# Optimization experiments

Hardware: AMD Instinct MI355X
Metric: run time of the kernel (lower is better)

## Reference

```python
import jax, jax.numpy as jnp
import numpy as np

DIM = 192
HRES, WRES = 64, 64
NUM_HEADS = 6
WS = 8  # window_size
MLP_HIDDEN = int(DIM * 4.0)
EPS = 1e-5


def layer_norm(x, gamma, beta):
    mu = jnp.mean(x, axis=-1, keepdims=True)
    var = jnp.var(x, axis=-1, keepdims=True)
    return (x - mu) * jax.lax.rsqrt(var + EPS) * gamma + beta


def window_partition(x, ws):
    B, H, W, C = x.shape
    x = x.reshape(B, H // ws, ws, W // ws, ws, C)
    x = jnp.transpose(x, (0, 1, 3, 2, 4, 5))
    return x.reshape(-1, ws * ws, C)


def window_reverse(windows, ws, H, W, C):
    B = windows.shape[0] // ((H // ws) * (W // ws))
    x = windows.reshape(B, H // ws, W // ws, ws, ws, C)
    x = jnp.transpose(x, (0, 1, 3, 2, 4, 5))
    return x.reshape(B, H, W, C)


def setup_inputs() -> dict:
    key = jax.random.key(0)
    ks = jax.random.split(key, 12)
    s = 0.02
    return {
        "x": jax.random.normal(ks[0], (32, HRES * WRES, DIM), dtype=jnp.float32),
        "norm1_g": jnp.ones((DIM,), jnp.float32),
        "norm1_b": jnp.zeros((DIM,), jnp.float32),
        "qkv_w": jax.random.normal(ks[1], (DIM, 3 * DIM), jnp.float32) * s,
        "qkv_b": jnp.zeros((3 * DIM,), jnp.float32),
        "proj_w": jax.random.normal(ks[2], (DIM, DIM), jnp.float32) * s,
        "proj_b": jnp.zeros((DIM,), jnp.float32),
        "norm2_g": jnp.ones((DIM,), jnp.float32),
        "norm2_b": jnp.zeros((DIM,), jnp.float32),
        "fc1_w": jax.random.normal(ks[3], (DIM, MLP_HIDDEN), jnp.float32) * s,
        "fc1_b": jnp.zeros((MLP_HIDDEN,), jnp.float32),
        "fc2_w": jax.random.normal(ks[4], (MLP_HIDDEN, DIM), jnp.float32) * s,
        "fc2_b": jnp.zeros((DIM,), jnp.float32),
    }


def reference(x, norm1_g, norm1_b, qkv_w, qkv_b, proj_w, proj_b,
              norm2_g, norm2_b, fc1_w, fc1_b, fc2_w, fc2_b):
    B, L, C = x.shape
    H, W = HRES, WRES
    hd = C // NUM_HEADS
    scale = hd ** -0.5

    shortcut = x
    h = layer_norm(x, norm1_g, norm1_b).reshape(B, H, W, C)
    win = window_partition(h, WS)  # [nW*B, WS*WS, C]
    Bw, N, _ = win.shape

    qkv = (win @ qkv_w + qkv_b).reshape(Bw, N, 3, NUM_HEADS, hd)
    q, k, v = jnp.transpose(qkv, (2, 0, 3, 1, 4))  # each [Bw, H, N, hd]
    attn = jnp.einsum('bhnd,bhmd->bhnm', q, k) * scale
    attn = jax.nn.softmax(attn, axis=-1)
    out = jnp.einsum('bhnm,bhmd->bhnd', attn, v)
    out = jnp.transpose(out, (0, 2, 1, 3)).reshape(Bw, N, C)
    out = out @ proj_w + proj_b

    h = window_reverse(out, WS, H, W, C).reshape(B, L, C)
    x = shortcut + h

    m = layer_norm(x, norm2_g, norm2_b)
    m = jax.nn.gelu(m @ fc1_w + fc1_b, approximate=False)
    m = m @ fc2_w + fc2_b
    return x + m
```

## Files before the change

### kernel.cpp

```cpp
#include <hip/hip_runtime.h>
#include <hip/hip_bf16.h>
#include <math.h>

#define DIM   192
#define NH    6
#define HD    32
#define WSZ   8
#define HRES_ 64
#define WRES_ 64
#define BATCH 32
#define LTOK  (HRES_*WRES_)
#define MTOK  (BATCH*LTOK)
#define QKVN  (3*DIM)
#define MLPH  (4*DIM)

using bf16 = __hip_bfloat16;
using bf16x8 = __attribute__((ext_vector_type(8))) short;
using f32x4  = __attribute__((ext_vector_type(4))) float;

__device__ __forceinline__ float bf2f(bf16 h) { return __bfloat162float(h); }
__device__ __forceinline__ float us2f(unsigned short u) {
    union { unsigned u32; float f; } c; c.u32 = ((unsigned)u) << 16; return c.f;
}

__global__ void detect_kernel(const unsigned short* __restrict__ g, int* __restrict__ flag)
{
    *flag = (g[0] == 0x3F80) ? 0 : 1;
}

__global__ __launch_bounds__(256) void cvt_kernel(
    const void* __restrict__ src, bf16* __restrict__ dst,
    long n, long elem_off, const int* __restrict__ flag)
{
    long i = ((long)blockIdx.x * 256 + threadIdx.x) * 8;
    if (i >= n) return;
    if (i + 8 <= n) {
        if (*flag) {
            const float* s = (const float*)src + elem_off + i;
            float4 a = *reinterpret_cast<const float4*>(s);
            float4 b = *reinterpret_cast<const float4*>(s + 4);
            bf16 o[8];
            o[0]=__float2bfloat16(a.x); o[1]=__float2bfloat16(a.y);
            o[2]=__float2bfloat16(a.z); o[3]=__float2bfloat16(a.w);
            o[4]=__float2bfloat16(b.x); o[5]=__float2bfloat16(b.y);
            o[6]=__float2bfloat16(b.z); o[7]=__float2bfloat16(b.w);
            *reinterpret_cast<bf16x8*>(dst + i) = *reinterpret_cast<const bf16x8*>(o);
        } else {
            *reinterpret_cast<bf16x8*>(dst + i) =
                *reinterpret_cast<const bf16x8*>((const bf16*)src + elem_off + i);
        }
    } else {
        for (long k2 = i; k2 < n; ++k2) {
            if (*flag) dst[k2] = __float2bfloat16(((const float*)src)[elem_off + k2]);
            else       dst[k2] = ((const bf16*)src)[elem_off + k2];
        }
    }
}

__global__ __launch_bounds__(256) void store_kernel(
    const bf16* __restrict__ src, void* __restrict__ dst,
    long n, long elem_off, const int* __restrict__ flag)
{
    long i = ((long)blockIdx.x * 256 + threadIdx.x) * 8;
    if (i >= n) return;
    if (i + 8 <= n) {
        bf16x8 v = *reinterpret_cast<const bf16x8*>(src + i);
        if (*flag) {
            float* d = (float*)dst + elem_off + i;
            float4 a, b;
            a.x = us2f((unsigned short)v[0]); a.y = us2f((unsigned short)v[1]);
            a.z = us2f((unsigned short)v[2]); a.w = us2f((unsigned short)v[3]);
            b.x = us2f((unsigned short)v[4]); b.y = us2f((unsigned short)v[5]);
            b.z = us2f((unsigned short)v[6]); b.w = us2f((unsigned short)v[7]);
            *reinterpret_cast<float4*>(d)     = a;
            *reinterpret_cast<float4*>(d + 4) = b;
        } else {
            *reinterpret_cast<bf16x8*>((bf16*)dst + elem_off + i) = v;
        }
    } else {
        for (long k2 = i; k2 < n; ++k2) {
            if (*flag) ((float*)dst)[elem_off + k2] = bf2f(src[k2]);
            else       ((bf16*)dst)[elem_off + k2] = src[k2];
        }
    }
}

__global__ __launch_bounds__(256) void ln_kernel(
    const bf16* __restrict__ x, const bf16* __restrict__ g,
    const bf16* __restrict__ b, bf16* __restrict__ y)
{
    int wave = threadIdx.x >> 6;
    int lane = threadIdx.x & 63;
    long token = (long)blockIdx.x * 4 + wave;
    const bf16* xp = x + token * DIM;
    float f0 = bf2f(xp[lane]);
    float f1 = bf2f(xp[lane + 64]);
    float f2 = bf2f(xp[lane + 128]);
    float s  = f0 + f1 + f2;
    float ss = f0*f0 + f1*f1 + f2*f2;
    #pragma unroll
    for (int m = 1; m < 64; m <<= 1) { s += __shfl_xor(s, m); ss += __shfl_xor(ss, m); }
    float mean = s * (1.0f/192.0f);
    float var  = ss * (1.0f/192.0f) - mean*mean;
    float rstd = rsqrtf(var + 1e-5f);
    bf16* yp = y + token * DIM;
    yp[lane]       = __float2bfloat16((f0-mean)*rstd*bf2f(g[lane])       + bf2f(b[lane]));
    yp[lane + 64]  = __float2bfloat16((f1-mean)*rstd*bf2f(g[lane + 64])  + bf2f(b[lane + 64]));
    yp[lane + 128] = __float2bfloat16((f2-mean)*rstd*bf2f(g[lane + 128]) + bf2f(b[lane + 128]));
}

__global__ void transpose_kernel(const bf16* __restrict__ in, bf16* __restrict__ out,
                                 int K, int N)
{
    int idx = blockIdx.x * 256 + threadIdx.x;
    if (idx < K * N) {
        int n = idx % N, k = idx / N;
        out[n * K + k] = in[idx];
    }
}

template<int EPI>
__global__ __launch_bounds__(256) void gemm_bt(
    const bf16* __restrict__ A, const bf16* __restrict__ Bt,
    const bf16* __restrict__ bias, const bf16* __restrict__ res,
    bf16* __restrict__ C, int M, int N, int K)
{
    constexpr int KC = 192;
    __shared__ __align__(16) bf16 bsh[(KC/32) * 4 * 64 * 8];
    int tid  = threadIdx.x;
    int wave = tid >> 6, lane = tid & 63;
    int t = lane & 15, q = lane >> 4;
    int  n0 = blockIdx.x * 64;
    long m0 = (long)blockIdx.y * 128;

    f32x4 acc[2][4] = {};

    for (int kc = 0; kc < K; kc += KC) {
        __syncthreads();
        for (int s = tid; s < (KC/32) * 256; s += 256) {
            int ks  = s >> 8;
            int rem = s & 255;
            int j   = rem >> 6;
            int ln  = rem & 63;
            int tt = ln & 15, qq = ln >> 4;
            int n = j * 16 + tt;
            int k = ks * 32 + qq * 8;
            const float4* src = reinterpret_cast<const float4*>(
                Bt + (long)(n0 + n) * K + kc + k);
            reinterpret_cast<float4*>(bsh)[s] = *src;
        }
        __syncthreads();

        const bf16* arow = A + (m0 + wave * 32 + t) * (long)K + kc + q * 8;
        #pragma unroll
        for (int ks = 0; ks < KC/32; ++ks) {
            bf16x8 a0 = *reinterpret_cast<const bf16x8*>(arow + ks * 32);
            bf16x8 a1 = *reinterpret_cast<const bf16x8*>(arow + 16 * (long)K + ks * 32);
            #pragma unroll
            for (int j = 0; j < 4; ++j) {
                bf16x8 b = reinterpret_cast<const bf16x8*>(bsh)[ks * 256 + j * 64 + lane];
                acc[0][j] = __builtin_amdgcn_mfma_f32_16x16x32_bf16(a0, b, acc[0][j], 0, 0, 0);
                acc[1][j] = __builtin_amdgcn_mfma_f32_16x16x32_bf16(a1, b, acc[1][j], 0, 0, 0);
            }
        }
    }

    #pragma unroll
    for (int j = 0; j < 4; ++j) {
        int col = n0 + j * 16 + t;
        float bv = bf2f(bias[col]);
        #pragma unroll
        for (int i = 0; i < 2; ++i) {
            #pragma unroll
            for (int r = 0; r < 4; ++r) {
                long row = m0 + wave * 32 + i * 16 + q * 4 + r;
                float v = acc[i][j][r] + bv;
                if (EPI == 1) v = v * 0.5f * (1.0f + erff(v * 0.70710678118f));
                if (EPI == 2) v += bf2f(res[row * N + col]);
                C[row * N + col] = __float2bfloat16(v);
            }
        }
    }
}

__global__ __launch_bounds__(256) void mlp_kernel(
    const bf16* __restrict__ A,   const bf16* __restrict__ W1t,
    const bf16* __restrict__ b1,  const bf16* __restrict__ W2t,
    const bf16* __restrict__ b2,  const bf16* __restrict__ res,
    bf16* __restrict__ out, int M)
{
    constexpr int HS = 88;
    __shared__ __align__(16) bf16 bsh[1536 * 8];
    __shared__ __align__(16) bf16 hsh[128 * HS];
    int tid  = threadIdx.x;
    int wave = tid >> 6, lane = tid & 63;
    int t = lane & 15, q = lane >> 4;
    long m0 = (long)blockIdx.x * 128;

    bf16x8 a_reg[2][6];
    #pragma unroll
    for (int i = 0; i < 2; ++i) {
        const bf16* ap = A + (m0 + wave * 32 + i * 16 + t) * (long)DIM + q * 8;
        #pragma unroll
        for (int ks = 0; ks < 6; ++ks)
            a_reg[i][ks] = *reinterpret_cast<const bf16x8*>(ap + ks * 32);
    }

    f32x4 oacc[2][12] = {};

    for (int nc = 0; nc < 12; ++nc) {
        __syncthreads();
        #pragma unroll
        for (int it = 0; it < 6; ++it) {
            int s   = it * 256 + tid;
            int ks  = s >> 8;
            int rem = s & 255;
            int j   = rem >> 6;
            int ln  = rem & 63;
            int n   = nc * 64 + j * 16 + (ln & 15);
            int k   = ks * 32 + (ln >> 4) * 8;
            reinterpret_cast<float4*>(bsh)[s] =
                *reinterpret_cast<const float4*>(W1t + (long)n * DIM + k);
        }
        __syncthreads();

        f32x4 hacc[2][4] = {};
        #pragma unroll
        for (int ks = 0; ks < 6; ++ks) {
            #pragma unroll
            for (int j = 0; j < 4; ++j) {
                bf16x8 b = reinterpret_cast<const bf16x8*>(bsh)[ks * 256 + j * 64 + lane];
                hacc[0][j] = __builtin_amdgcn_mfma_f32_16x16x32_bf16(a_reg[0][ks], b, hacc[0][j], 0, 0, 0);
                hacc[1][j] = __builtin_amdgcn_mfma_f32_16x16x32_bf16(a_reg[1][ks], b, hacc[1][j], 0, 0, 0);
            }
        }
        #pragma unroll
        for (int j = 0; j < 4; ++j) {
            float bv = bf2f(b1[nc * 64 + j * 16 + t]);
            #pragma unroll
            for (int i = 0; i < 2; ++i) {
                #pragma unroll
                for (int r = 0; r < 4; ++r) {
                    int row = wave * 32 + i * 16 + q * 4 + r;
                    float v = hacc[i][j][r] + bv;
                    v = v * 0.5f * (1.0f + erff(v * 0.70710678118f));
                    hsh[row * HS + j * 16 + t] = __float2bfloat16(v);
                }
            }
        }
        __syncthreads();

        #pragma unroll
        for (int it = 0; it < 6; ++it) {
            int s   = it * 256 + tid;
            int ks  = s / 768;
            int rem = s - ks * 768;
            int j   = rem >> 6;
            int ln  = rem & 63;
            int n   = j * 16 + (ln & 15);
            int k   = nc * 64 + ks * 32 + (ln >> 4) * 8;
            reinterpret_cast<float4*>(bsh)[s] =
                *reinterpret_cast<const float4*>(W2t + (long)n * MLPH + k);
        }
        __syncthreads();

        #pragma unroll
        for (int ks = 0; ks < 2; ++ks) {
            bf16x8 h0 = *reinterpret_cast<const bf16x8*>(hsh + (wave * 32 + t) * HS + ks * 32 + q * 8);
            bf16x8 h1 = *reinterpret_cast<const bf16x8*>(hsh + (wave * 32 + 16 + t) * HS + ks * 32 + q * 8);
            #pragma unroll
            for (int j = 0; j < 12; ++j) {
                bf16x8 b = reinterpret_cast<const bf16x8*>(bsh)[ks * 768 + j * 64 + lane];
                oacc[0][j] = __builtin_amdgcn_mfma_f32_16x16x32_bf16(h0, b, oacc[0][j], 0, 0, 0);
                oacc[1][j] = __builtin_amdgcn_mfma_f32_16x16x32_bf16(h1, b, oacc[1][j], 0, 0, 0);
            }
        }
    }

    #pragma unroll
    for (int j = 0; j < 12; ++j) {
        int col = j * 16 + t;
        float bv = bf2f(b2[col]);
        #pragma unroll
        for (int i = 0; i < 2; ++i) {
            #pragma unroll
            for (int r = 0; r < 4; ++r) {
                long row = m0 + wave * 32 + i * 16 + q * 4 + r;
                float v = oacc[i][j][r] + bv + bf2f(res[row * DIM + col]);
                out[row * DIM + col] = __float2bfloat16(v);
            }
        }
    }
}

__global__ __launch_bounds__(256) void attn_kernel(
    const bf16* __restrict__ qkv, bf16* __restrict__ out)
{
    int win  = blockIdx.x;
    int head = blockIdx.y;
    __shared__ __align__(16) bf16 qs[64 * 32];
    __shared__ __align__(16) bf16 ksm[64 * 32];
    __shared__ __align__(16) bf16 vt[32 * 64];
    __shared__ __align__(16) bf16 ps[64 * 64];
    __shared__ int nat[64];

    int tid  = threadIdx.x;
    int wave = tid >> 6, lane = tid & 63;
    int t = lane & 15, q = lane >> 4;

    if (tid < 64) {
        int b = win >> 6;
        int widx = win & 63;
        int wh = widx >> 3, ww = widx & 7;
        int r = wh * 8 + (tid >> 3);
        int c = ww * 8 + (tid & 7);
        nat[tid] = b * LTOK + r * WRES_ + c;
    }
    __syncthreads();

    {
        int token = tid >> 2, ch = tid & 3;
        long base = (long)nat[token] * QKVN + head * HD + ch * 8;
        float4 qv = *reinterpret_cast<const float4*>(qkv + base);
        float4 kv = *reinterpret_cast<const float4*>(qkv + base + DIM);
        float4 vv = *reinterpret_cast<const float4*>(qkv + base + 2 * DIM);
        *reinterpret_cast<float4*>(qs  + token * 32 + ch * 8) = qv;
        *reinterpret_cast<float4*>(ksm + token * 32 + ch * 8) = kv;
        const bf16* vp = reinterpret_cast<const bf16*>(&vv);
        #pragma unroll
        for (int e = 0; e < 8; ++e) vt[(ch * 8 + e) * 64 + token] = vp[e];
    }
    __syncthreads();

    f32x4 sacc[4] = {};
    {
        bf16x8 aq = *reinterpret_cast<const bf16x8*>(qs + (wave * 16 + t) * 32 + q * 8);
        #pragma unroll
        for (int j = 0; j < 4; ++j) {
            bf16x8 bk = *reinterpret_cast<const bf16x8*>(ksm + (j * 16 + t) * 32 + q * 8);
            sacc[j] = __builtin_amdgcn_mfma_f32_16x16x32_bf16(aq, bk, sacc[j], 0, 0, 0);
        }
    }

    const float scale = 0.17677669529663689f;
    #pragma unroll
    for (int r = 0; r < 4; ++r) {
        float m_ = fmaxf(fmaxf(sacc[0][r], sacc[1][r]), fmaxf(sacc[2][r], sacc[3][r]));
        #pragma unroll
        for (int msk = 1; msk < 16; msk <<= 1) m_ = fmaxf(m_, __shfl_xor(m_, msk));
        float p[4], sum = 0.f;
        #pragma unroll
        for (int j = 0; j < 4; ++j) { p[j] = expf((sacc[j][r] - m_) * scale); sum += p[j]; }
        #pragma unroll
        for (int msk = 1; msk < 16; msk <<= 1) sum += __shfl_xor(sum, msk);
        float inv = 1.0f / sum;
        int row = wave * 16 + q * 4 + r;
        #pragma unroll
        for (int j = 0; j < 4; ++j)
            ps[row * 64 + j * 16 + t] = __float2bfloat16(p[j] * inv);
    }
    __syncthreads();

    f32x4 oacc[2] = {};
    #pragma unroll
    for (int kk = 0; kk < 2; ++kk) {
        bf16x8 ap = *reinterpret_cast<const bf16x8*>(ps + (wave * 16 + t) * 64 + kk * 32 + q * 8);
        #pragma unroll
        for (int j = 0; j < 2; ++j) {
            bf16x8 bv = *reinterpret_cast<const bf16x8*>(vt + (j * 16 + t) * 64 + kk * 32 + q * 8);
            oacc[j] = __builtin_amdgcn_mfma_f32_16x16x32_bf16(ap, bv, oacc[j], 0, 0, 0);
        }
    }
    #pragma unroll
    for (int j = 0; j < 2; ++j) {
        #pragma unroll
        for (int r = 0; r < 4; ++r) {
            int row = wave * 16 + q * 4 + r;
            out[(long)nat[row] * DIM + head * HD + j * 16 + t] = __float2bfloat16(oacc[j][r]);
        }
    }
}

extern "C" void kernel_launch(void* const* d_in, const int* in_sizes, int n_in,
                              void* d_out, int out_size, void* d_ws, size_t ws_size,
                              hipStream_t stream)
{
    char* ws = (char*)d_ws;
    size_t off = 0;
    auto alloc = [&](size_t bytes) {
        char* p = ws + off;
        off += (bytes + 255) & ~(size_t)255;
        return p;
    };

    int* flag = (int*)alloc(sizeof(int));

    static const int psz[12] = { DIM, DIM, DIM*QKVN, QKVN, DIM*DIM, DIM,
                                 DIM, DIM, DIM*MLPH, MLPH, MLPH*DIM, DIM };
    bf16* par[12];
    for (int i = 0; i < 12; ++i) par[i] = (bf16*)alloc((size_t)psz[i] * 2);
    bf16 *n1g = par[0], *n1b = par[1], *qkvw = par[2], *qkvb = par[3],
         *projw = par[4], *projb = par[5], *n2g = par[6], *n2b = par[7],
         *fc1w = par[8], *fc1b = par[9], *fc2w = par[10], *fc2b = par[11];

    bf16* wqkv_t  = (bf16*)alloc((size_t)QKVN * DIM * 2);
    bf16* wproj_t = (bf16*)alloc((size_t)DIM * DIM * 2);
    bf16* wfc1_t  = (bf16*)alloc((size_t)MLPH * DIM * 2);
    bf16* wfc2_t  = (bf16*)alloc((size_t)DIM * MLPH * 2);
    size_t fixed_off = off;

    int C = 32;
    while (C > 1) {
        size_t Mc = (size_t)C * LTOK;
        if (fixed_off + Mc * 2304 + 4096 <= ws_size) break;
        C >>= 1;
    }
    size_t Mc = (size_t)C * LTOK;
    bf16* xb = (bf16*)alloc(Mc * 384);
    bf16* R  = (bf16*)alloc(Mc * 384);
    bf16* Y  = (bf16*)alloc(Mc * 384);
    bf16* S  = (bf16*)alloc(Mc * 1152);
    int nchunks = BATCH / C;

    detect_kernel<<<1, 1, 0, stream>>>((const unsigned short*)d_in[1], flag);

    for (int i = 0; i < 12; ++i) {
        unsigned blocks = (unsigned)(((long)psz[i] + 8*256 - 1) / (8*256));
        cvt_kernel<<<blocks, 256, 0, stream>>>(d_in[i + 1], par[i], psz[i], 0, flag);
    }

    transpose_kernel<<<(DIM*QKVN + 255)/256, 256, 0, stream>>>(qkvw, wqkv_t, DIM, QKVN);
    transpose_kernel<<<(DIM*DIM  + 255)/256, 256, 0, stream>>>(projw, wproj_t, DIM, DIM);
    transpose_kernel<<<(DIM*MLPH + 255)/256, 256, 0, stream>>>(fc1w, wfc1_t, DIM, MLPH);
    transpose_kernel<<<(MLPH*DIM + 255)/256, 256, 0, stream>>>(fc2w, wfc2_t, MLPH, DIM);

    for (int ci = 0; ci < nchunks; ++ci) {
        long eoff = (long)ci * Mc * DIM;
        long nelem = (long)Mc * DIM;
        unsigned vblocks = (unsigned)((nelem + 8*256 - 1) / (8*256));

        cvt_kernel<<<vblocks, 256, 0, stream>>>(d_in[0], xb, nelem, eoff, flag);
        ln_kernel<<<(unsigned)(Mc/4), 256, 0, stream>>>(xb, n1g, n1b, R);
        gemm_bt<0><<<dim3(QKVN/64, Mc/128), 256, 0, stream>>>(R, wqkv_t, qkvb, nullptr, S, (int)Mc, QKVN, DIM);
        attn_kernel<<<dim3(C*64, NH), 256, 0, stream>>>(S, R);
        gemm_bt<2><<<dim3(DIM/64, Mc/128), 256, 0, stream>>>(R, wproj_t, projb, xb, Y, (int)Mc, DIM, DIM);
        ln_kernel<<<(unsigned)(Mc/4), 256, 0, stream>>>(Y, n2g, n2b, R);
        mlp_kernel<<<(unsigned)(Mc/128), 256, 0, stream>>>(R, wfc1_t, fc1b, wfc2_t, fc2b, Y, Y, (int)Mc);
        store_kernel<<<vblocks, 256, 0, stream>>>(Y, d_out, nelem, eoff, flag);
    }
}
```

Measured before the change: 791.9 us.

## Halve MLP kernel row tile to 64 rows for higher occupancy

The fused MLP kernel now processes 64 rows per block instead of 128, each wave handling one 16-row MFMA tile instead of two. Accumulators, A registers and the hidden shared buffer shrink, and launch bounds request 3 blocks per CU, aiming to raise occupancy and latency hiding. In exchange, each block reloads the full fc1/fc2 weights for half as many rows, doubling weight traffic through shared memory and halving MFMA reuse per B-fragment load.

New measurement: 714.4 us. 1.11x faster.

```diff
diff --git a/kernel.cpp b/kernel.cpp
--- a/kernel.cpp
+++ b/kernel.cpp
@@ -183,7 +183,7 @@
     }
 }
 
-__global__ __launch_bounds__(256) void mlp_kernel(
+__global__ __launch_bounds__(256, 3) void mlp_kernel(
     const bf16* __restrict__ A,   const bf16* __restrict__ W1t,
     const bf16* __restrict__ b1,  const bf16* __restrict__ W2t,
     const bf16* __restrict__ b2,  const bf16* __restrict__ res,
@@ -191,22 +191,21 @@
 {
     constexpr int HS = 88;
     __shared__ __align__(16) bf16 bsh[1536 * 8];
-    __shared__ __align__(16) bf16 hsh[128 * HS];
+    __shared__ __align__(16) bf16 hsh[64 * HS];
     int tid  = threadIdx.x;
     int wave = tid >> 6, lane = tid & 63;
     int t = lane & 15, q = lane >> 4;
-    long m0 = (long)blockIdx.x * 128;
-
-    bf16x8 a_reg[2][6];
-    #pragma unroll
-    for (int i = 0; i < 2; ++i) {
-        const bf16* ap = A + (m0 + wave * 32 + i * 16 + t) * (long)DIM + q * 8;
+    long m0 = (long)blockIdx.x * 64;
+
+    bf16x8 a_reg[6];
+    {
+        const bf16* ap = A + (m0 + wave * 16 + t) * (long)DIM + q * 8;
         #pragma unroll
         for (int ks = 0; ks < 6; ++ks)
-            a_reg[i][ks] = *reinterpret_cast<const bf16x8*>(ap + ks * 32);
-    }
-
-    f32x4 oacc[2][12] = {};
+            a_reg[ks] = *reinterpret_cast<const bf16x8*>(ap + ks * 32);
+    }
+
+    f32x4 oacc[12] = {};
 
     for (int nc = 0; nc < 12; ++nc) {
         __syncthreads();
@@ -224,28 +223,24 @@
         }
         __syncthreads();
 
-        f32x4 hacc[2][4] = {};
+        f32x4 hacc[4] = {};
         #pragma unroll
         for (int ks = 0; ks < 6; ++ks) {
             #pragma unroll
             for (int j = 0; j < 4; ++j) {
                 bf16x8 b = reinterpret_cast<const bf16x8*>(bsh)[ks * 256 + j * 64 + lane];
-                hacc[0][j] = __builtin_amdgcn_mfma_f32_16x16x32_bf16(a_reg[0][ks], b, hacc[0][j], 0, 0, 0);
-                hacc[1][j] = __builtin_amdgcn_mfma_f32_16x16x32_bf16(a_reg[1][ks], b, hacc[1][j], 0, 0, 0);
+                hacc[j] = __builtin_amdgcn_mfma_f32_16x16x32_bf16(a_reg[ks], b, hacc[j], 0, 0, 0);
             }
         }
         #pragma unroll
         for (int j = 0; j < 4; ++j) {
             float bv = bf2f(b1[nc * 64 + j * 16 + t]);
             #pragma unroll
-            for (int i = 0; i < 2; ++i) {
-                #pragma unroll
-                for (int r = 0; r < 4; ++r) {
-                    int row = wave * 32 + i * 16 + q * 4 + r;
-                    float v = hacc[i][j][r] + bv;
-                    v = v * 0.5f * (1.0f + erff(v * 0.70710678118f));
-                    hsh[row * HS + j * 16 + t] = __float2bfloat16(v);
-                }
+            for (int r = 0; r < 4; ++r) {
+                int row = wave * 16 + q * 4 + r;
+                float v = hacc[j][r] + bv;
+                v = v * 0.5f * (1.0f + erff(v * 0.70710678118f));
+                hsh[row * HS + j * 16 + t] = __float2bfloat16(v);
             }
         }
         __syncthreads();
@@ -266,13 +261,11 @@
 
         #pragma unroll
         for (int ks = 0; ks < 2; ++ks) {
-            bf16x8 h0 = *reinterpret_cast<const bf16x8*>(hsh + (wave * 32 + t) * HS + ks * 32 + q * 8);
-            bf16x8 h1 = *reinterpret_cast<const bf16x8*>(hsh + (wave * 32 + 16 + t) * HS + ks * 32 + q * 8);
+            bf16x8 h = *reinterpret_cast<const bf16x8*>(hsh + (wave * 16 + t) * HS + ks * 32 + q * 8);
             #pragma unroll
             for (int j = 0; j < 12; ++j) {
                 bf16x8 b = reinterpret_cast<const bf16x8*>(bsh)[ks * 768 + j * 64 + lane];
-                oacc[0][j] = __builtin_amdgcn_mfma_f32_16x16x32_bf16(h0, b, oacc[0][j], 0, 0, 0);
-                oacc[1][j] = __builtin_amdgcn_mfma_f32_16x16x32_bf16(h1, b, oacc[1][j], 0, 0, 0);
+                oacc[j] = __builtin_amdgcn_mfma_f32_16x16x32_bf16(h, b, oacc[j], 0, 0, 0);
             }
         }
     }
@@ -282,13 +275,10 @@
         int col = j * 16 + t;
         float bv = bf2f(b2[col]);
         #pragma unroll
-        for (int i = 0; i < 2; ++i) {
-            #pragma unroll
-            for (int r = 0; r < 4; ++r) {
-                long row = m0 + wave * 32 + i * 16 + q * 4 + r;
-                float v = oacc[i][j][r] + bv + bf2f(res[row * DIM + col]);
-                out[row * DIM + col] = __float2bfloat16(v);
-            }
+        for (int r = 0; r < 4; ++r) {
+            long row = m0 + wave * 16 + q * 4 + r;
+            float v = oacc[j][r] + bv + bf2f(res[row * DIM + col]);
+            out[row * DIM + col] = __float2bfloat16(v);
         }
     }
 }
@@ -445,7 +435,7 @@
         attn_kernel<<<dim3(C*64, NH), 256, 0, stream>>>(S, R);
         gemm_bt<2><<<dim3(DIM/64, Mc/128), 256, 0, stream>>>(R, wproj_t, projb, xb, Y, (int)Mc, DIM, DIM);
         ln_kernel<<<(unsigned)(Mc/4), 256, 0, stream>>>(Y, n2g, n2b, R);
-        mlp_kernel<<<(unsigned)(Mc/128), 256, 0, stream>>>(R, wfc1_t, fc1b, wfc2_t, fc2b, Y, Y, (int)Mc);
+        mlp_kernel<<<(unsigned)(Mc/64), 256, 0, stream>>>(R, wfc1_t, fc1b, wfc2_t, fc2b, Y, Y, (int)Mc);
         store_kernel<<<vblocks, 256, 0, stream>>>(Y, d_out, nelem, eoff, flag);
     }
 }
```

## Split fused MLP block into 64-row tile with 2x2 wave grid

Applied to the files above, without the earlier changes.

Halves the fused MLP kernel's row tile from 128 to 64 and arranges the four waves as a 2x2 grid, so each wave computes half the hidden columns and half the output columns. This cuts the accumulator registers per wave (oacc drops from 24 to 12 vectors) and adds a launch bound asking for 3 blocks per SM, to raise occupancy and double the block count. In exchange, each fc1/fc2 weight tile staged in shared memory is reused across only 64 rows, which doubles total weight traffic from L2 into LDS.

Result: faster. 753.6 us (-4.8%).

```diff
diff --git a/kernel.cpp b/kernel.cpp
--- a/kernel.cpp
+++ b/kernel.cpp
@@ -22,6 +22,7 @@
 __device__ __forceinline__ float us2f(unsigned short u) {
     union { unsigned u32; float f; } c; c.u32 = ((unsigned)u) << 16; return c.f;
 }
+
 
 __global__ void detect_kernel(const unsigned short* __restrict__ g, int* __restrict__ flag)
 {
@@ -183,7 +184,7 @@
     }
 }
 
-__global__ __launch_bounds__(256) void mlp_kernel(
+__global__ __launch_bounds__(256, 3) void mlp_kernel(
     const bf16* __restrict__ A,   const bf16* __restrict__ W1t,
     const bf16* __restrict__ b1,  const bf16* __restrict__ W2t,
     const bf16* __restrict__ b2,  const bf16* __restrict__ res,
@@ -191,22 +192,23 @@
 {
     constexpr int HS = 88;
     __shared__ __align__(16) bf16 bsh[1536 * 8];
-    __shared__ __align__(16) bf16 hsh[128 * HS];
+    __shared__ __align__(16) bf16 hsh[64 * HS];
     int tid  = threadIdx.x;
     int wave = tid >> 6, lane = tid & 63;
     int t = lane & 15, q = lane >> 4;
-    long m0 = (long)blockIdx.x * 128;
+    int wr = wave >> 1, wc = wave & 1;
+    long m0 = (long)blockIdx.x * 64;
 
     bf16x8 a_reg[2][6];
     #pragma unroll
     for (int i = 0; i < 2; ++i) {
-        const bf16* ap = A + (m0 + wave * 32 + i * 16 + t) * (long)DIM + q * 8;
+        const bf16* ap = A + (m0 + wr * 32 + i * 16 + t) * (long)DIM + q * 8;
         #pragma unroll
         for (int ks = 0; ks < 6; ++ks)
             a_reg[i][ks] = *reinterpret_cast<const bf16x8*>(ap + ks * 32);
     }
 
-    f32x4 oacc[2][12] = {};
+    f32x4 oacc[2][6] = {};
 
     for (int nc = 0; nc < 12; ++nc) {
         __syncthreads();
@@ -224,27 +226,28 @@
         }
         __syncthreads();
 
-        f32x4 hacc[2][4] = {};
+        f32x4 hacc[2][2] = {};
         #pragma unroll
         for (int ks = 0; ks < 6; ++ks) {
-            #pragma unroll
-            for (int j = 0; j < 4; ++j) {
-                bf16x8 b = reinterpret_cast<const bf16x8*>(bsh)[ks * 256 + j * 64 + lane];
-                hacc[0][j] = __builtin_amdgcn_mfma_f32_16x16x32_bf16(a_reg[0][ks], b, hacc[0][j], 0, 0, 0);
-                hacc[1][j] = __builtin_amdgcn_mfma_f32_16x16x32_bf16(a_reg[1][ks], b, hacc[1][j], 0, 0, 0);
-            }
-        }
-        #pragma unroll
-        for (int j = 0; j < 4; ++j) {
-            float bv = bf2f(b1[nc * 64 + j * 16 + t]);
+            bf16x8 b0 = reinterpret_cast<const bf16x8*>(bsh)[ks * 256 + (wc * 2 + 0) * 64 + lane];
+            bf16x8 b1v = reinterpret_cast<const bf16x8*>(bsh)[ks * 256 + (wc * 2 + 1) * 64 + lane];
+            hacc[0][0] = __builtin_amdgcn_mfma_f32_16x16x32_bf16(a_reg[0][ks], b0,  hacc[0][0], 0, 0, 0);
+            hacc[0][1] = __builtin_amdgcn_mfma_f32_16x16x32_bf16(a_reg[0][ks], b1v, hacc[0][1], 0, 0, 0);
+            hacc[1][0] = __builtin_amdgcn_mfma_f32_16x16x32_bf16(a_reg[1][ks], b0,  hacc[1][0], 0, 0, 0);
+            hacc[1][1] = __builtin_amdgcn_mfma_f32_16x16x32_bf16(a_reg[1][ks], b1v, hacc[1][1], 0, 0, 0);
+        }
+        #pragma unroll
+        for (int j = 0; j < 2; ++j) {
+            int col = wc * 32 + j * 16 + t;
+            float bv = bf2f(b1[nc * 64 + col]);
             #pragma unroll
             for (int i = 0; i < 2; ++i) {
                 #pragma unroll
                 for (int r = 0; r < 4; ++r) {
-                    int row = wave * 32 + i * 16 + q * 4 + r;
+                    int row = wr * 32 + i * 16 + q * 4 + r;
                     float v = hacc[i][j][r] + bv;
                     v = v * 0.5f * (1.0f + erff(v * 0.70710678118f));
-                    hsh[row * HS + j * 16 + t] = __float2bfloat16(v);
+                    hsh[row * HS + col] = __float2bfloat16(v);
                 }
             }
         }
@@ -266,11 +269,11 @@
 
         #pragma unroll
         for (int ks = 0; ks < 2; ++ks) {
-            bf16x8 h0 = *reinterpret_cast<const bf16x8*>(hsh + (wave * 32 + t) * HS + ks * 32 + q * 8);
-            bf16x8 h1 = *reinterpret_cast<const bf16x8*>(hsh + (wave * 32 + 16 + t) * HS + ks * 32 + q * 8);
+            bf16x8 h0 = *reinterpret_cast<const bf16x8*>(hsh + (wr * 32 + t) * HS + ks * 32 + q * 8);
+            bf16x8 h1 = *reinterpret_cast<const bf16x8*>(hsh + (wr * 32 + 16 + t) * HS + ks * 32 + q * 8);
             #pragma unroll
-            for (int j = 0; j < 12; ++j) {
-                bf16x8 b = reinterpret_cast<const bf16x8*>(bsh)[ks * 768 + j * 64 + lane];
+            for (int j = 0; j < 6; ++j) {
+                bf16x8 b = reinterpret_cast<const bf16x8*>(bsh)[ks * 768 + (wc * 6 + j) * 64 + lane];
                 oacc[0][j] = __builtin_amdgcn_mfma_f32_16x16x32_bf16(h0, b, oacc[0][j], 0, 0, 0);
                 oacc[1][j] = __builtin_amdgcn_mfma_f32_16x16x32_bf16(h1, b, oacc[1][j], 0, 0, 0);
             }
@@ -278,14 +281,14 @@
     }
 
     #pragma unroll
-    for (int j = 0; j < 12; ++j) {
-        int col = j * 16 + t;
+    for (int j = 0; j < 6; ++j) {
+        int col = wc * 96 + j * 16 + t;
         float bv = bf2f(b2[col]);
         #pragma unroll
         for (int i = 0; i < 2; ++i) {
             #pragma unroll
             for (int r = 0; r < 4; ++r) {
-                long row = m0 + wave * 32 + i * 16 + q * 4 + r;
+                long row = m0 + wr * 32 + i * 16 + q * 4 + r;
                 float v = oacc[i][j][r] + bv + bf2f(res[row * DIM + col]);
                 out[row * DIM + col] = __float2bfloat16(v);
             }
@@ -445,7 +448,7 @@
         attn_kernel<<<dim3(C*64, NH), 256, 0, stream>>>(S, R);
         gemm_bt<2><<<dim3(DIM/64, Mc/128), 256, 0, stream>>>(R, wproj_t, projb, xb, Y, (int)Mc, DIM, DIM);
         ln_kernel<<<(unsigned)(Mc/4), 256, 0, stream>>>(Y, n2g, n2b, R);
-        mlp_kernel<<<(unsigned)(Mc/128), 256, 0, stream>>>(R, wfc1_t, fc1b, wfc2_t, fc2b, Y, Y, (int)Mc);
+        mlp_kernel<<<(unsigned)(Mc/64), 256, 0, stream>>>(R, wfc1_t, fc1b, wfc2_t, fc2b, Y, Y, (int)Mc);
         store_kernel<<<vblocks, 256, 0, stream>>>(Y, d_out, nelem, eoff, flag);
     }
 }
```
